# Kernel tuning notes

Hardware: AMD Instinct MI355X
Metric: run time of the kernel (lower is better)

Reference implementation:

```python
import jax, jax.numpy as jnp
import numpy as np


def _run_stacked_lstm(x, init_hc, params):
    """x: [B,T,E]; init_hc: tuple of (h,c) per layer; params: tuple of (W,U,b) per layer.
    Keras LSTMCell gate order: i, f, g(candidate), o; sigmoid recurrent act, tanh act."""
    def step(carry, xt):
        inp = xt
        new = []
        for (h, c), (W, U, b) in zip(carry, params):
            z = inp @ W + h @ U + b                      # [B, 4*units]
            i, f, g, o = jnp.split(z, 4, axis=-1)
            c2 = jax.nn.sigmoid(f) * c + jax.nn.sigmoid(i) * jnp.tanh(g)
            h2 = jax.nn.sigmoid(o) * jnp.tanh(c2)
            new.append((h2, c2))
            inp = h2                                     # feed to next layer
        return tuple(new), inp
    carry, ys = jax.lax.scan(step, init_hc, jnp.swapaxes(x, 0, 1))
    return jnp.swapaxes(ys, 0, 1), carry                 # [B,T,units], final states


def setup_inputs() -> dict:
    key = jax.random.key(0)
    ks = jax.random.split(key, 20)
    B, T, V, E, H, L = 16, 64, 32000, 512, 512, 2
    s = 0.02
    inp = {
        'ids_1': jax.random.randint(ks[0], (B, T), 0, V),
        'ids_2': jax.random.randint(ks[1], (B, T), 0, V),
        'init_state': jax.random.normal(ks[2], (L, B, H), jnp.float32),
        'emb': jax.random.normal(ks[3], (V, E), jnp.float32) * s,
        'W1_0': jax.random.normal(ks[4], (E, 4 * H), jnp.float32) * s,
        'U1_0': jax.random.normal(ks[5], (H, 4 * H), jnp.float32) * s,
        'b1_0': jnp.zeros((4 * H,), jnp.float32),
        'W1_1': jax.random.normal(ks[6], (H, 4 * H), jnp.float32) * s,
        'U1_1': jax.random.normal(ks[7], (H, 4 * H), jnp.float32) * s,
        'b1_1': jnp.zeros((4 * H,), jnp.float32),
        'W2_0': jax.random.normal(ks[8], (E, 8 * H), jnp.float32) * s,
        'U2_0': jax.random.normal(ks[9], (2 * H, 8 * H), jnp.float32) * s,
        'b2_0': jnp.zeros((8 * H,), jnp.float32),
        'W2_1': jax.random.normal(ks[10], (2 * H, 8 * H), jnp.float32) * s,
        'U2_1': jax.random.normal(ks[11], (2 * H, 8 * H), jnp.float32) * s,
        'b2_1': jnp.zeros((8 * H,), jnp.float32),
        'Wp1': jax.random.normal(ks[12], (H, V), jnp.float32) * s,
        'bp1': jnp.zeros((V,), jnp.float32),
        'Wp2': jax.random.normal(ks[13], (2 * H, V), jnp.float32) * s,
        'bp2': jnp.zeros((V,), jnp.float32),
    }
    return inp


def reference(ids_1, ids_2, init_state, emb,
              W1_0, U1_0, b1_0, W1_1, U1_1, b1_1,
              W2_0, U2_0, b2_0, W2_1, U2_1, b2_1,
              Wp1, bp1, Wp2, bp2):
    L = init_state.shape[0]
    e1 = emb[ids_1]                                       # [B,T,E]
    e2 = emb[ids_2]
    # RNN1: initial (h,c) both set to init_state per layer
    init1 = tuple((init_state[l], init_state[l]) for l in range(L))
    p1 = ((W1_0, U1_0, b1_0), (W1_1, U1_1, b1_1))
    out1, st1 = _run_stacked_lstm(e1, init1, p1)
    logits1 = out1 @ Wp1 + bp1                            # [B,T,V]
    # RNN2: initial h = concat(init, h1_final), c = concat(init, c1_final)
    init2 = tuple((jnp.concatenate([init_state[l], st1[l][0]], axis=1),
                   jnp.concatenate([init_state[l], st1[l][1]], axis=1))
                  for l in range(L))
    p2 = ((W2_0, U2_0, b2_0), (W2_1, U2_1, b2_1))
    out2, _ = _run_stacked_lstm(e2, init2, p2)
    logits2 = out2 @ Wp2 + bp2                            # [B,T,V]
    return (logits1, logits2)
```

## Files before the change

### kernel.cpp

```cpp
#include <hip/hip_runtime.h>
#include <hip/hip_bf16.h>

#define B_ 16
#define T_ 64
#define E_ 512
#define H_ 512
#define V_ 32000

typedef __attribute__((ext_vector_type(4))) float f32x4;
typedef __attribute__((ext_vector_type(8))) short s16x8;

__device__ __forceinline__ float sigm(float x){ return 1.0f/(1.0f + __expf(-x)); }

__device__ __forceinline__ unsigned short f2bf(float x){
  unsigned int u = __float_as_uint(x);
  return (unsigned short)((u + 0x7FFFu + ((u>>16)&1u)) >> 16);
}

__device__ __forceinline__ unsigned load_coh(const unsigned* p){
  unsigned v;
  asm volatile("global_load_dword %0, %1, off sc0 sc1\n\ts_waitcnt vmcnt(0)"
               : "=v"(v) : "v"(p) : "memory");
  return v;
}
__device__ __forceinline__ void store_coh16(unsigned short* p, unsigned v){
  asm volatile("global_store_short %0, %1, off sc0 sc1" :: "v"(p), "v"(v) : "memory");
}
__device__ __forceinline__ void store_cohf(float* p, float v){
  asm volatile("global_store_dword %0, %1, off sc0 sc1" :: "v"(p), "v"(v) : "memory");
}
__device__ __forceinline__ void store_cohu(unsigned* p, unsigned v){
  asm volatile("global_store_dword %0, %1, off sc0 sc1" :: "v"(p), "v"(v) : "memory");
}

__device__ __forceinline__ void gbar3(unsigned* barb, unsigned bi1, int nblk,
                                      bool det, int myblk){
  asm volatile("s_waitcnt vmcnt(0)" ::: "memory");
  __syncthreads();
  const int tid = threadIdx.x;
  if(tid == 0) store_cohu(barb + (size_t)myblk*16, bi1);
  if(det){
    if(tid < nblk){
      const unsigned* fp = barb + (size_t)tid*16;
      while(load_coh(fp) < bi1) __builtin_amdgcn_s_sleep(1);
    }
    __syncthreads();
    if(tid < 8) store_cohu(barb + 4096 + (size_t)tid*16, bi1);
  } else {
    if(tid == 0){
      const unsigned* gp = barb + 4096 + (size_t)(myblk & 7)*16;
      while(load_coh(gp) < bi1) __builtin_amdgcn_s_sleep(1);
    }
  }
  __syncthreads();
}

__global__ void k_barinit(unsigned* bar){
  int i = blockIdx.x*256 + threadIdx.x;
  if(i < 16384) bar[i] = 0u;
}

__global__ void k_gather(const int* __restrict__ ids, const float* __restrict__ emb,
                         unsigned short* __restrict__ out){
  const int row = blockIdx.x;
  const int id  = ids[row];
  float4 v = *(const float4*)(emb + (size_t)id*E_ + threadIdx.x*4);
  ushort4 o;
  o.x = f2bf(v.x); o.y = f2bf(v.y); o.z = f2bf(v.z); o.w = f2bf(v.w);
  *(ushort4*)(out + (size_t)row*E_ + threadIdx.x*4) = o;
}

__device__ __forceinline__ void tcvt_dev(const float* __restrict__ in,
    unsigned short* __restrict__ out, int N, int Hp, int Kfull, int koff, int swz,
    int bx, int by, float (*tile)[33]){
  const int n0 = bx*32, k0 = by*32;
  const int x = threadIdx.x & 31, y = threadIdx.x >> 5;
  __syncthreads();
  #pragma unroll
  for(int i=0;i<4;i++){
    int k = y + i*8;
    tile[k][x] = in[(size_t)(k0+k)*N + n0 + x];
  }
  __syncthreads();
  #pragma unroll
  for(int i=0;i<4;i++){
    int nl = y + i*8;
    int n  = n0 + nl;
    int p  = Hp ? ((n % Hp)*4 + n / Hp) : n;
    int kk = koff + k0 + x;
    size_t idx;
    if(swz){
      int k2 = kk*2;
      int slot = ((k2>>4)&7) ^ (p&7);
      idx = (size_t)p*Kfull + (((k2 & ~127) | (slot<<4) | (k2 & 15)) >> 1);
    } else {
      idx = (size_t)p*Kfull + kk;
    }
    out[idx] = f2bf(tile[x][nl]);
  }
}

__global__ __launch_bounds__(256)
void k_tcvt(const float* __restrict__ in, unsigned short* __restrict__ out,
            int N, int Hp, int Kfull, int koff, int swz){
  __shared__ float tile[32][33];
  tcvt_dev(in, out, N, Hp, Kfull, koff, swz, blockIdx.x, blockIdx.y, tile);
}

__device__ __forceinline__ void tcvtw_dev(const float* __restrict__ in,
    unsigned short* __restrict__ out, int N, int K, int bx, int by,
    float (*tile)[257]){
  const int tid = threadIdx.x;
  const int n0 = bx*256, k0 = by*32;
  const int row = tid >> 3, nc = (tid & 7)*32;
  __syncthreads();
  #pragma unroll
  for(int j=0;j<8;j++){
    float4 v = *(const float4*)(in + (size_t)(k0+row)*N + n0 + nc + j*4);
    *(float4*)&tile[row][nc + j*4] = v;
  }
  __syncthreads();
  __align__(16) unsigned short vals[32];
  #pragma unroll
  for(int k=0;k<32;k++) vals[k] = f2bf(tile[k][tid]);
  unsigned short* op = out + (size_t)(n0+tid)*K + k0;
  #pragma unroll
  for(int j=0;j<4;j++)
    *(uint4*)(op + j*8) = *(const uint4*)&vals[j*8];
}

__global__ void k_bpack(const float* __restrict__ b, float* __restrict__ out, int H, int N){
  int p = blockIdx.x*256 + threadIdx.x;
  if(p < N) out[p] = b[(p&3)*H + (p>>2)];
}

__global__ void k_init1(const float* __restrict__ init_state,
                        unsigned short* h0i, float* c0i, unsigned short* h1i, float* c1i){
  int i = blockIdx.x*256 + threadIdx.x;
  if(i >= B_*H_) return;
  float v0 = init_state[i];
  float v1 = init_state[B_*H_ + i];
  h0i[i] = f2bf(v0); c0i[i] = v0;
  h1i[i] = f2bf(v1); c1i[i] = v1;
}

__global__ void k_init2(const float* __restrict__ init_state,
                        const unsigned short* __restrict__ h0seq1,
                        const unsigned short* __restrict__ h1seq1,
                        const float* __restrict__ c0f1, const float* __restrict__ c1f1,
                        unsigned short* h20i, unsigned short* h21i,
                        float* c20i, float* c21i){
  const int l = blockIdx.y;
  int i = blockIdx.x*256 + threadIdx.x;
  if(i >= B_*2*H_) return;
  const int r = i >> 10, j = i & 1023;
  unsigned short* ho = l ? h21i : h20i;
  float* co = l ? c21i : c20i;
  if(j < H_){
    float v = init_state[(size_t)l*B_*H_ + r*H_ + j];
    ho[i] = f2bf(v); co[i] = v;
  } else {
    const unsigned short* hs = l ? h1seq1 : h0seq1;
    const float* cf = l ? c1f1 : c0f1;
    ho[i] = hs[(size_t)((T_-1)*B_ + r)*H_ + (j - H_)];
    co[i] = cf[r*H_ + (j - H_)];
  }
}

__device__ __forceinline__ void mm_tile(const unsigned short* __restrict__ A,
    const unsigned short* __restrict__ Bt, const float* __restrict__ bias,
    float* __restrict__ C, int N, int K, int bm, int bn,
    unsigned short* As, unsigned short* Bs, int remap){
  const int tid = threadIdx.x;
  const int lane = tid & 63, w = tid >> 6;
  const int wm = (w>>1)*64, wn = (w&1)*64;
  const int l15 = lane & 15, kg = lane >> 4;
  f32x4 acc[4][4] = {};
  for(int k0=0; k0<K; k0+=64){
    __syncthreads();
    #pragma unroll
    for(int ch=0; ch<4; ch++){
      int off = ch*4096 + tid*16;
      int row = off >> 7;
      int s   = ((off >> 4) & 7) ^ (row & 7);
      __builtin_amdgcn_global_load_lds(
        (const __attribute__((address_space(1))) unsigned int*)(A + (size_t)(bm+row)*K + k0 + s*8),
        (__attribute__((address_space(3))) unsigned int*)((char*)As + off), 16, 0, 0);
    }
    #pragma unroll
    for(int ch=0; ch<4; ch++){
      int off = ch*4096 + tid*16;
      int row = off >> 7;
      int s   = ((off >> 4) & 7) ^ (row & 7);
      __builtin_amdgcn_global_load_lds(
        (const __attribute__((address_space(1))) unsigned int*)(Bt + (size_t)(bn+row)*K + k0 + s*8),
        (__attribute__((address_space(3))) unsigned int*)((char*)Bs + off), 16, 0, 0);
    }
    __syncthreads();
    #pragma unroll
    for(int q=0;q<2;q++){
      s16x8 af[4], bf[4];
      #pragma unroll
      for(int mt=0;mt<4;mt++){
        int row = wm + mt*16 + l15;
        int s = (q*4 + kg) ^ (row & 7);
        af[mt] = *(const s16x8*)(As + row*64 + s*8);
      }
      #pragma unroll
      for(int nt=0;nt<4;nt++){
        int row = wn + nt*16 + l15;
        int s = (q*4 + kg) ^ (row & 7);
        bf[nt] = *(const s16x8*)(Bs + row*64 + s*8);
      }
      #pragma unroll
      for(int mt=0;mt<4;mt++)
        #pragma unroll
        for(int nt=0;nt<4;nt++)
          acc[mt][nt] = __builtin_amdgcn_mfma_f32_16x16x32_bf16(af[mt], bf[nt], acc[mt][nt], 0, 0, 0);
    }
  }
  #pragma unroll
  for(int mt=0;mt<4;mt++){
    #pragma unroll
    for(int nt=0;nt<4;nt++){
      int col = bn + wn + nt*16 + l15;
      float bv = bias ? bias[col] : 0.f;
      #pragma unroll
      for(int e=0;e<4;e++){
        int row = bm + wm + mt*16 + kg*4 + e;
        int orow = remap ? ((row & 15)*T_ + (row >> 4)) : row;
        C[(size_t)orow*N + col] = acc[mt][nt][e] + bv;
      }
    }
  }
}

template<int BF32>
__global__ __launch_bounds__(256)
void k_mm(const unsigned short* __restrict__ A, const void* __restrict__ Bsrc,
          const float* __restrict__ bias, float* __restrict__ C,
          int M, int N, int K, int remap, int bm0){
  __shared__ __align__(16) unsigned short As[128*64];
  __shared__ __align__(16) unsigned short Bs[128*64];
  if(!BF32){
    mm_tile(A, (const unsigned short*)Bsrc, bias, C, N, K,
            bm0 + blockIdx.y*128, blockIdx.x*128, As, Bs, remap);
    return;
  }
  const int tid = threadIdx.x;
  const int lane = tid & 63, w = tid >> 6;
  const int wm = (w>>1)*64, wn = (w&1)*64;
  const int bm = bm0 + blockIdx.y*128, bn = blockIdx.x*128;
  const int l15 = lane & 15, kg = lane >> 4;
  f32x4 acc[4][4] = {};
  for(int k0=0; k0<K; k0+=64){
    __syncthreads();
    #pragma unroll
    for(int ch=0; ch<4; ch++){
      int off = ch*4096 + tid*16;
      int row = off >> 7;
      int s   = ((off >> 4) & 7) ^ (row & 7);
      __builtin_amdgcn_global_load_lds(
        (const __attribute__((address_space(1))) unsigned int*)(A + (size_t)(bm+row)*K + k0 + s*8),
        (__attribute__((address_space(3))) unsigned int*)((char*)As + off), 16, 0, 0);
    }
    {
      const float* Bf = (const float*)Bsrc;
      #pragma unroll
      for(int i=0;i<8;i++){
        int kl = (tid>>5) + i*8;
        int nl = (tid&31)*4;
        float4 v = *(const float4*)(Bf + (size_t)(k0+kl)*N + bn + nl);
        int slot = kl >> 3, kb = kl & 7;
        float vv[4] = {v.x, v.y, v.z, v.w};
        #pragma unroll
        for(int jj=0;jj<4;jj++){
          int n = nl + jj;
          Bs[n*64 + ((slot ^ (n&7))*8) + kb] = f2bf(vv[jj]);
        }
      }
    }
    __syncthreads();
    #pragma unroll
    for(int q=0;q<2;q++){
      s16x8 af[4], bf[4];
      #pragma unroll
      for(int mt=0;mt<4;mt++){
        int row = wm + mt*16 + l15;
        int s = (q*4 + kg) ^ (row & 7);
        af[mt] = *(const s16x8*)(As + row*64 + s*8);
      }
      #pragma unroll
      for(int nt=0;nt<4;nt++){
        int row = wn + nt*16 + l15;
        int s = (q*4 + kg) ^ (row & 7);
        bf[nt] = *(const s16x8*)(Bs + row*64 + s*8);
      }
      #pragma unroll
      for(int mt=0;mt<4;mt++)
        #pragma unroll
        for(int nt=0;nt<4;nt++)
          acc[mt][nt] = __builtin_amdgcn_mfma_f32_16x16x32_bf16(af[mt], bf[nt], acc[mt][nt], 0, 0, 0);
    }
  }
  #pragma unroll
  for(int mt=0;mt<4;mt++){
    #pragma unroll
    for(int nt=0;nt<4;nt++){
      int col = bn + wn + nt*16 + l15;
      float bv = bias ? bias[col] : 0.f;
      #pragma unroll
      for(int e=0;e<4;e++){
        int row = bm + wm + mt*16 + kg*4 + e;
        int orow = remap ? ((row & 15)*T_ + (row >> 4)) : row;
        C[(size_t)orow*N + col] = acc[mt][nt][e] + bv;
      }
    }
  }
}

template<int C, int K, int LAYER, int HU, int TB>
__device__ __forceinline__ void rnn_body(
    unsigned short* __restrict__ Uld, float* __restrict__ zp,
    const unsigned short* __restrict__ Uslice,
    const float* __restrict__ xw0, const float* __restrict__ bpk,
    const unsigned short* __restrict__ h0init, const unsigned short* __restrict__ h1init,
    const float* __restrict__ cinit,
    unsigned short* __restrict__ h0seq, unsigned short* __restrict__ h1seq,
    float* __restrict__ cfin, unsigned* bar, int cb, int nblk, bool det, int myblk)
{
  constexpr int KW = K/4, KS = KW/32, FR = C/16, UB = C/4;
  constexpr int K2 = K*2;
  constexpr int ITEMS = 16*UB;
  const int tid = threadIdx.x;
  const int lane = tid & 63, w = tid >> 6;
  const int l15 = lane & 15, kg = lane >> 4;

  constexpr int CP = (C*K2)/4096;
  #pragma unroll
  for(int i=0;i<CP;i++){
    __builtin_amdgcn_global_load_lds(
      (const __attribute__((address_space(1))) unsigned int*)((const char*)Uslice + i*4096 + tid*16),
      (__attribute__((address_space(3))) unsigned int*)((char*)Uld + i*4096 + tid*16), 16, 0, 0);
  }
  const int base_p = cb*C;
  const int base_u = cb*UB;
  float4 bvr = make_float4(0.f,0.f,0.f,0.f);
  int er = 0, eu = 0;
  if(tid < ITEMS){ er = tid / UB; eu = tid - er*UB; bvr = *(const float4*)(bpk + base_p + eu*4); }
  float creg = 0.f;
  unsigned short* hseqW = LAYER ? h1seq : h0seq;

  int cbyte[FR], cx[FR];
  #pragma unroll
  for(int f=0;f<FR;f++){ int c = f*16 + l15; cbyte[f] = c*K2; cx[f] = (c&7)<<4; }

  __syncthreads();

  for(int it = 0; it <= T_; ++it){
    const bool active = LAYER ? (it >= 1) : (it < T_);
    const int t = LAYER ? it-1 : it;
    if(active){
      const unsigned short* asrc;
      if constexpr(LAYER == 0){
        asrc = (t == 0) ? (h0init + l15*HU)
             : (h0seq + ((size_t)(TB ? ((t-1)*B_ + l15) : (l15*T_ + (t-1))))*HU);
      } else {
        if(w < 2){
          asrc = h0seq + ((size_t)(TB ? (t*B_ + l15) : (l15*T_ + t)))*HU;
        } else {
          asrc = ((t == 0) ? (h1init + l15*HU)
               : (h1seq + ((size_t)(TB ? ((t-1)*B_ + l15) : (l15*T_ + (t-1))))*HU)) - HU;
        }
      }
      f32x4 acc[FR];
      #pragma unroll
      for(int f=0;f<FR;f++) acc[f] = (f32x4){0.f,0.f,0.f,0.f};
      #pragma unroll
      for(int s=0;s<KS;s++){
        const int kel = w*KW + s*32 + kg*8;
        s16x8 a = *(const s16x8*)(asrc + kel);
        const int kb  = kel*2;
        const int kch = kb & ~127;
        const int ksl = (kb >> 4) & 7;
        #pragma unroll
        for(int f=0;f<FR;f++){
          const int ad = cbyte[f] + kch + ((ksl<<4) ^ cx[f]);
          s16x8 b = *(const s16x8*)((const char*)Uld + ad);
          acc[f] = __builtin_amdgcn_mfma_f32_16x16x32_bf16(a, b, acc[f], 0, 0, 0);
        }
      }
      #pragma unroll
      for(int f=0;f<FR;f++)
        #pragma unroll
        for(int e=0;e<4;e++)
          zp[(w*16 + kg*4 + e)*68 + f*16 + l15] = acc[f][e];
    }
    __syncthreads();
    if(active && tid < ITEMS){
      float4 z0 = *(const float4*)(zp + (     er)*68 + eu*4);
      float4 z1 = *(const float4*)(zp + (16 + er)*68 + eu*4);
      float4 z2 = *(const float4*)(zp + (32 + er)*68 + eu*4);
      float4 z3 = *(const float4*)(zp + (48 + er)*68 + eu*4);
      float si = z0.x+z1.x+z2.x+z3.x + bvr.x;
      float sf = z0.y+z1.y+z2.y+z3.y + bvr.y;
      float sg = z0.z+z1.z+z2.z+z3.z + bvr.z;
      float so = z0.w+z1.w+z2.w+z3.w + bvr.w;
      if constexpr(LAYER == 0){
        float4 xv = *(const float4*)(xw0 + ((size_t)(er*T_ + t))*(4*HU) + base_p + eu*4);
        si += xv.x; sf += xv.y; sg += xv.z; so += xv.w;
      }
      float cin = (t == 0) ? cinit[er*HU + base_u + eu] : creg;
      float c2 = sigm(sf)*cin + sigm(si)*tanhf(sg);
      float h2 = sigm(so)*tanhf(c2);
      creg = c2;
      size_t hrow = TB ? ((size_t)(t*B_ + er)) : ((size_t)(er*T_ + t));
      store_coh16(&hseqW[hrow*HU + base_u + eu], (unsigned)f2bf(h2));
      if(t == T_-1) store_cohf(&cfin[er*HU + base_u + eu], c2);
    }
    if(it < T_) gbar3(bar, (unsigned)(it+1), nblk, det, myblk);
  }
  asm volatile("s_waitcnt vmcnt(0)" ::: "memory");
  __syncthreads();
  if(tid == 0) store_cohu(bar + (size_t)myblk*16, (unsigned)(T_+1));
}

__global__ __launch_bounds__(256, 1)
void k_rnn1m(const unsigned short* __restrict__ Ut0, const unsigned short* __restrict__ WU1,
    const float* __restrict__ xw0, const float* __restrict__ bpk0, const float* __restrict__ bpk1,
    const unsigned short* __restrict__ h0init, const unsigned short* __restrict__ h1init,
    const float* __restrict__ c0init, const float* __restrict__ c1init,
    unsigned short* __restrict__ h0seq, unsigned short* __restrict__ h1seq,
    float* __restrict__ c0fin, float* __restrict__ c1fin, unsigned* bar,
    const int* __restrict__ ids2, const float* __restrict__ emb, unsigned short* __restrict__ ebuf2,
    const float* __restrict__ b2_0, const float* __restrict__ b2_1,
    float* __restrict__ bpk20, float* __restrict__ bpk21,
    const float* __restrict__ U2_0, unsigned short* __restrict__ ut0_2,
    const float* __restrict__ W2_0, unsigned short* __restrict__ wtmp2,
    const float* __restrict__ W2_1, const float* __restrict__ U2_1, unsigned short* __restrict__ wu1_2,
    const float* __restrict__ Wp1, unsigned short* __restrict__ wpT1,
    const float* __restrict__ Wp2, unsigned short* __restrict__ wpT2,
    const float* __restrict__ bp1, float* __restrict__ out1,
    float* __restrict__ xw2buf, int wide)
{
  constexpr int HU = 512, C0 = 64, C1 = 64;
  constexpr int NB0 = 4*HU/C0;
  constexpr int NRNN = NB0 + 4*HU/C1;
  constexpr int NP = 96;
  constexpr int NJ = 96;
  __shared__ __align__(16) unsigned short Uld[65536];
  __shared__ __align__(16) float zred[64*68];
  const int blk = blockIdx.x;
  const int tid = threadIdx.x;
  if(blk < NB0){
    rnn_body<C0, HU, 0, HU, 1>(Uld, zred, Ut0 + (size_t)blk*C0*HU, xw0, bpk0,
        h0init, h1init, c0init, h0seq, h1seq, c0fin, bar, blk, NRNN, blk==0, blk);
  } else if(blk < NRNN){
    rnn_body<C1, 2*HU, 1, HU, 1>(Uld, zred, WU1 + (size_t)(blk-NB0)*C1*2*HU, nullptr, bpk1,
        h0init, h1init, c1init, h0seq, h1seq, c1fin, bar, blk-NB0, NRNN, false, blk);
  } else if(blk < NRNN + NP){
    const int q = blk - NRNN;
    float (*tile)[33]   = (float(*)[33])Uld;
    float (*tile2)[257] = (float(*)[257])Uld;
    unsigned short* As = Uld;
    unsigned short* Bs = Uld + 8192;
    if(wide){
      for(int j = q; j < 2000; j += NP)
        tcvtw_dev(Wp1, wpT1, 32000, 512, j%125, j/125, tile2);
    }
    __syncthreads();
    __threadfence();
    if(tid == 0)
      __hip_atomic_fetch_add(bar + 5136, 1u, __ATOMIC_RELAXED, __HIP_MEMORY_SCOPE_AGENT);
    const int J0 = 512, J1 = J0+32, J2 = J1+4096, J3 = J2+2048, J4 = J3+4096, J5 = J4+4096;
    const int J6 = wide ? (J5 + 4000) : J5;
    for(int j = q; j < J6; j += NP){
      if(j < J0){
        int row = j*2 + (tid>>7);
        int id = ids2[row];
        float4 v = *(const float4*)(emb + (size_t)id*E_ + (tid&127)*4);
        ushort4 o; o.x=f2bf(v.x); o.y=f2bf(v.y); o.z=f2bf(v.z); o.w=f2bf(v.w);
        *(ushort4*)(ebuf2 + (size_t)row*E_ + (tid&127)*4) = o;
      } else if(j < J1){
        int jj = j - J0;
        const float* b = (jj < 16) ? b2_0 : b2_1;
        float* o = (jj < 16) ? bpk20 : bpk21;
        int p = (jj & 15)*256 + tid;
        o[p] = b[(p&3)*1024 + (p>>2)];
      } else if(j < J2){
        int r = j - J1; tcvt_dev(U2_0, ut0_2, 4096, 1024, 1024, 0, 1, r%128, r/128, tile);
      } else if(j < J3){
        int r = j - J2; tcvt_dev(W2_0, wtmp2, 4096, 1024, 512, 0, 0, r%128, r/128, tile);
      } else if(j < J4){
        int r = j - J3; tcvt_dev(W2_1, wu1_2, 4096, 1024, 2048, 0, 1, r%128, r/128, tile);
      } else if(j < J5){
        int r = j - J4; tcvt_dev(U2_1, wu1_2, 4096, 1024, 2048, 1024, 1, r%128, r/128, tile);
      } else {
        int r = j - J5; tcvtw_dev(Wp2, wpT2, 32000, 1024, r%125, r/125, tile2);
      }
    }
    __syncthreads();
    __threadfence();
    if(tid == 0)
      __hip_atomic_fetch_add(bar + 5152, 1u, __ATOMIC_RELAXED, __HIP_MEMORY_SCOPE_AGENT);
    if(tid == 0){
      while(load_coh(bar + 5152) < (unsigned)NP) __builtin_amdgcn_s_sleep(8);
    }
    __syncthreads();
    if(xw2buf){
      for(int t2 = q; t2 < 256; t2 += NP)
        mm_tile(ebuf2, wtmp2, nullptr, xw2buf, 4096, 512, (t2>>5)*128, (t2&31)*128, As, Bs, 0);
    }
  } else {
    if(!wide) return;
    const int q2 = blk - NRNN - NP;
    unsigned short* As = Uld;
    unsigned short* Bs = Uld + 8192;
    volatile int* rdy = (volatile int*)((char*)Uld + 128000);
    if(tid == 0){
      while(load_coh(bar + 5136) < (unsigned)NP) __builtin_amdgcn_s_sleep(8);
    }
    __syncthreads();
    for(int g = 0; g < 8; ++g){
      const unsigned req = 8u*(unsigned)g + 9u;
      for(;;){
        if(tid == 0) *rdy = 1;
        __syncthreads();
        if(tid < 32){
          if(load_coh(bar + (size_t)(NB0 + tid)*16) < req) *rdy = 0;
        }
        __syncthreads();
        if(*rdy) break;
        __builtin_amdgcn_s_sleep(16);
      }
      for(int n = q2; n < 250; n += NJ)
        mm_tile(h1seq, wpT1, bp1, out1, V_, 512, g*128, n*128, As, Bs, 1);
    }
  }
}

template<int HU, int C0, int C1>
__global__ __launch_bounds__(256, 1)
void k_rnn(const unsigned short* __restrict__ Ut0, const unsigned short* __restrict__ WU1,
           const float* __restrict__ xw0, const float* __restrict__ bpk0, const float* __restrict__ bpk1,
           const unsigned short* __restrict__ h0init, const unsigned short* __restrict__ h1init,
           const float* __restrict__ c0init, const float* __restrict__ c1init,
           unsigned short* __restrict__ h0seq, unsigned short* __restrict__ h1seq,
           float* __restrict__ c0fin, float* __restrict__ c1fin, unsigned* bar)
{
  constexpr int NB0 = 4*HU/C0;
  constexpr int UMAXE = (C0*HU > C1*2*HU) ? C0*HU : C1*2*HU;
  __shared__ __align__(16) unsigned short Uld[UMAXE];
  __shared__ __align__(16) float zred[64*68];
  const int nblk = gridDim.x;
  const bool det = (blockIdx.x == 0);
  const int blk = blockIdx.x;
  if(blk < NB0)
    rnn_body<C0, HU, 0, HU, 1>(Uld, zred, Ut0 + (size_t)blk*C0*HU, xw0, bpk0,
                               h0init, h1init, c0init, h0seq, h1seq, c0fin, bar, blk, nblk, det, blk);
  else
    rnn_body<C1, 2*HU, 1, HU, 1>(Uld, zred, WU1 + (size_t)(blk-NB0)*C1*2*HU, nullptr, bpk1,
                               h0init, h1init, c1init, h0seq, h1seq, c1fin, bar, blk-NB0, nblk, det, blk);
}

extern "C" void kernel_launch(void* const* d_in, const int* in_sizes, int n_in,
                              void* d_out, int out_size, void* d_ws, size_t ws_size,
                              hipStream_t stream){
  const int*   ids1 = (const int*)d_in[0];
  const int*   ids2 = (const int*)d_in[1];
  const float* init = (const float*)d_in[2];
  const float* emb  = (const float*)d_in[3];
  const float* W1_0 = (const float*)d_in[4];
  const float* U1_0 = (const float*)d_in[5];
  const float* b1_0 = (const float*)d_in[6];
  const float* W1_1 = (const float*)d_in[7];
  const float* U1_1 = (const float*)d_in[8];
  const float* b1_1 = (const float*)d_in[9];
  const float* W2_0 = (const float*)d_in[10];
  const float* U2_0 = (const float*)d_in[11];
  const float* b2_0 = (const float*)d_in[12];
  const float* W2_1 = (const float*)d_in[13];
  const float* U2_1 = (const float*)d_in[14];
  const float* b2_1 = (const float*)d_in[15];
  const float* Wp1  = (const float*)d_in[16];
  const float* bp1  = (const float*)d_in[17];
  const float* Wp2  = (const float*)d_in[18];
  const float* bp2  = (const float*)d_in[19];
  float* out1 = (float*)d_out;
  float* out2 = out1 + (size_t)B_*T_*V_;

  char* base = (char*)d_ws;
  float*          xw    = (float*)(base);
  unsigned short* ut0_1 = (unsigned short*)(base + (16u<<20));
  unsigned short* wu1_1 = (unsigned short*)(base + (18u<<20));
  unsigned short* ut0_2 = (unsigned short*)(base + (22u<<20));
  unsigned short* wu1_2 = (unsigned short*)(base + (30u<<20));
  unsigned short* wtmp  = (unsigned short*)(base + (46u<<20));
  unsigned short* ebuf  = (unsigned short*)(base + (50u<<20));
  unsigned short* h0s1  = (unsigned short*)(base + (51u<<20));
  unsigned short* h1s1  = (unsigned short*)(base + (52u<<20));
  unsigned short* h0s2  = (unsigned short*)(base + (53u<<20));
  unsigned short* h1s2  = (unsigned short*)(base + (55u<<20));
  char* M = base + (57u<<20);
  unsigned short* h0i1 = (unsigned short*)(M);
  unsigned short* h1i1 = (unsigned short*)(M + 16384);
  float* c0i1 = (float*)(M + 32768);
  float* c1i1 = (float*)(M + 65536);
  unsigned short* h2i0 = (unsigned short*)(M + 98304);
  unsigned short* h2i1 = (unsigned short*)(M + 131072);
  float* c2i0 = (float*)(M + 163840);
  float* c2i1 = (float*)(M + 229376);
  float* c0f1 = (float*)(M + 294912);
  float* c1f1 = (float*)(M + 327680);
  float* c0f2 = (float*)(M + 360448);
  float* c1f2 = (float*)(M + 425984);
  float* bpk10 = (float*)(M + 491520);
  float* bpk11 = (float*)(M + 499712);
  float* bpk20 = (float*)(M + 507904);
  float* bpk21 = (float*)(M + 524288);
  unsigned* bar1 = (unsigned*)(M + 540672);
  unsigned* bar2 = (unsigned*)(M + 540672 + 32768);
  unsigned short* wpT1 = (unsigned short*)(base + (58u<<20));
  unsigned short* wpT2 = (unsigned short*)(base + (90u<<20));
  float*          xw2  = (float*)(base + (153u<<20));
  const size_t NEED_W  = ((size_t)90u<<20) + (size_t)V_*1024*2;
  const size_t NEED_W2 = ((size_t)169u<<20);
  const bool wide  = ws_size >= NEED_W;
  const bool wide2 = ws_size >= NEED_W2;
  float* xw2p = (wide && wide2) ? xw2 : xw;

  k_barinit<<<dim3(64), dim3(256), 0, stream>>>(bar1);

  k_init1<<<dim3(32), dim3(256), 0, stream>>>(init, h0i1, c0i1, h1i1, c1i1);
  k_gather<<<dim3(B_*T_), dim3(128), 0, stream>>>(ids1, emb, ebuf);
  k_tcvt<<<dim3(64, 16), dim3(256), 0, stream>>>(U1_0, ut0_1, 2048, 512, 512, 0, 1);
  k_tcvt<<<dim3(64, 16), dim3(256), 0, stream>>>(W1_0, wtmp,  2048, 512, 512, 0, 0);
  k_tcvt<<<dim3(64, 16), dim3(256), 0, stream>>>(W1_1, wu1_1, 2048, 512, 1024, 0, 1);
  k_tcvt<<<dim3(64, 16), dim3(256), 0, stream>>>(U1_1, wu1_1, 2048, 512, 1024, 512, 1);
  k_bpack<<<dim3(8),  dim3(256), 0, stream>>>(b1_0, bpk10, 512, 2048);
  k_bpack<<<dim3(8),  dim3(256), 0, stream>>>(b1_1, bpk11, 512, 2048);
  k_mm<0><<<dim3(16, 8), dim3(256), 0, stream>>>(ebuf, wtmp, nullptr, xw, 1024, 2048, 512, 0, 0);

  k_rnn1m<<<dim3(256), dim3(256), 0, stream>>>(ut0_1, wu1_1, xw, bpk10, bpk11,
      h0i1, h1i1, c0i1, c1i1, h0s1, h1s1, c0f1, c1f1, bar1,
      ids2, emb, ebuf, b2_0, b2_1, bpk20, bpk21,
      U2_0, ut0_2, W2_0, wtmp, W2_1, U2_1, wu1_2,
      Wp1, wpT1, Wp2, wpT2, bp1, out1,
      (wide && wide2) ? xw2 : nullptr, (int)wide);

  if(!wide){
    k_mm<1><<<dim3(250, 8), dim3(256), 0, stream>>>(h1s1, Wp1, bp1, out1, 1024, V_, 512, 1, 0);
  }
  if(!wide || !wide2){
    k_mm<0><<<dim3(32, 8), dim3(256), 0, stream>>>(ebuf, wtmp, nullptr, xw, 1024, 4096, 512, 0, 0);
  }
  k_init2<<<dim3(64, 2), dim3(256), 0, stream>>>(init, h0s1, h1s1, c0f1, c1f1,
                                                 h2i0, h2i1, c2i0, c2i1);

  k_rnn<1024, 64, 32><<<dim3(192), dim3(256), 0, stream>>>(ut0_2, wu1_2, xw2p, bpk20, bpk21,
      h2i0, h2i1, c2i0, c2i1, h0s2, h1s2, c0f2, c1f2, bar2);

  if(wide){
    k_mm<0><<<dim3(250, 8), dim3(256), 0, stream>>>(h1s2, wpT2, bp2, out2, 1024, V_, 1024, 1, 0);
  } else {
    k_mm<1><<<dim3(250, 8), dim3(256), 0, stream>>>(h1s2, Wp2, bp2, out2, 1024, V_, 1024, 1, 0);
  }
}
```

Baseline: 872.1 us.

## Replace centralized grid barrier with per-block flag polling and layer-scoped dependencies

Removes the two-level grid barrier, in which a detector block gathered all flags and then broadcast a release. Each RNN block now publishes its own step counter and, at the start of every step, polls the flags it depends on directly. Layer-0 blocks wait only on layer-0 blocks, while layer-1 blocks wait on all RNN blocks. This drops one hop of global-memory latency per step and loosens coupling between the layers, at the cost of more polling traffic from 64 threads per block.

```diff
diff --git a/kernel.cpp b/kernel.cpp
--- a/kernel.cpp
+++ b/kernel.cpp
@@ -31,28 +31,6 @@
 }
 __device__ __forceinline__ void store_cohu(unsigned* p, unsigned v){
   asm volatile("global_store_dword %0, %1, off sc0 sc1" :: "v"(p), "v"(v) : "memory");
-}
-
-__device__ __forceinline__ void gbar3(unsigned* barb, unsigned bi1, int nblk,
-                                      bool det, int myblk){
-  asm volatile("s_waitcnt vmcnt(0)" ::: "memory");
-  __syncthreads();
-  const int tid = threadIdx.x;
-  if(tid == 0) store_cohu(barb + (size_t)myblk*16, bi1);
-  if(det){
-    if(tid < nblk){
-      const unsigned* fp = barb + (size_t)tid*16;
-      while(load_coh(fp) < bi1) __builtin_amdgcn_s_sleep(1);
-    }
-    __syncthreads();
-    if(tid < 8) store_cohu(barb + 4096 + (size_t)tid*16, bi1);
-  } else {
-    if(tid == 0){
-      const unsigned* gp = barb + 4096 + (size_t)(myblk & 7)*16;
-      while(load_coh(gp) < bi1) __builtin_amdgcn_s_sleep(1);
-    }
-  }
-  __syncthreads();
 }
 
 __global__ void k_barinit(unsigned* bar){
@@ -327,7 +305,7 @@
     const unsigned short* __restrict__ h0init, const unsigned short* __restrict__ h1init,
     const float* __restrict__ cinit,
     unsigned short* __restrict__ h0seq, unsigned short* __restrict__ h1seq,
-    float* __restrict__ cfin, unsigned* bar, int cb, int nblk, bool det, int myblk)
+    float* __restrict__ cfin, unsigned* bar, int cb, int nb0, int nrnn, int myblk)
 {
   constexpr int KW = K/4, KS = KW/32, FR = C/16, UB = C/4;
   constexpr int K2 = K*2;
@@ -358,6 +336,18 @@
   __syncthreads();
 
   for(int it = 0; it <= T_; ++it){
+    if(it > 0){
+      if(tid < 64){
+        const int fmax = (LAYER == 0) ? nb0 : nrnn;
+        for(int f = tid; f < fmax; f += 64){
+          const unsigned* fp = bar + (size_t)f*16;
+          if(load_coh(fp) < (unsigned)it){
+            while(load_coh(fp) < (unsigned)it) __builtin_amdgcn_s_sleep(4);
+          }
+        }
+      }
+      __syncthreads();
+    }
     const bool active = LAYER ? (it >= 1) : (it < T_);
     const int t = LAYER ? it-1 : it;
     if(active){
@@ -418,11 +408,10 @@
       store_coh16(&hseqW[hrow*HU + base_u + eu], (unsigned)f2bf(h2));
       if(t == T_-1) store_cohf(&cfin[er*HU + base_u + eu], c2);
     }
-    if(it < T_) gbar3(bar, (unsigned)(it+1), nblk, det, myblk);
-  }
-  asm volatile("s_waitcnt vmcnt(0)" ::: "memory");
-  __syncthreads();
-  if(tid == 0) store_cohu(bar + (size_t)myblk*16, (unsigned)(T_+1));
+    asm volatile("s_waitcnt vmcnt(0)" ::: "memory");
+    __syncthreads();
+    if(tid == 0) store_cohu(bar + (size_t)myblk*16, (unsigned)(it+1));
+  }
 }
 
 __global__ __launch_bounds__(256, 1)
@@ -454,10 +443,10 @@
   const int tid = threadIdx.x;
   if(blk < NB0){
     rnn_body<C0, HU, 0, HU, 1>(Uld, zred, Ut0 + (size_t)blk*C0*HU, xw0, bpk0,
-        h0init, h1init, c0init, h0seq, h1seq, c0fin, bar, blk, NRNN, blk==0, blk);
+        h0init, h1init, c0init, h0seq, h1seq, c0fin, bar, blk, NB0, NRNN, blk);
   } else if(blk < NRNN){
     rnn_body<C1, 2*HU, 1, HU, 1>(Uld, zred, WU1 + (size_t)(blk-NB0)*C1*2*HU, nullptr, bpk1,
-        h0init, h1init, c1init, h0seq, h1seq, c1fin, bar, blk-NB0, NRNN, false, blk);
+        h0init, h1init, c1init, h0seq, h1seq, c1fin, bar, blk-NB0, NB0, NRNN, blk);
   } else if(blk < NRNN + NP){
     const int q = blk - NRNN;
     float (*tile)[33]   = (float(*)[33])Uld;
@@ -549,18 +538,17 @@
            float* __restrict__ c0fin, float* __restrict__ c1fin, unsigned* bar)
 {
   constexpr int NB0 = 4*HU/C0;
+  constexpr int NRNN = NB0 + 4*HU/C1;
   constexpr int UMAXE = (C0*HU > C1*2*HU) ? C0*HU : C1*2*HU;
   __shared__ __align__(16) unsigned short Uld[UMAXE];
   __shared__ __align__(16) float zred[64*68];
-  const int nblk = gridDim.x;
-  const bool det = (blockIdx.x == 0);
   const int blk = blockIdx.x;
   if(blk < NB0)
     rnn_body<C0, HU, 0, HU, 1>(Uld, zred, Ut0 + (size_t)blk*C0*HU, xw0, bpk0,
-                               h0init, h1init, c0init, h0seq, h1seq, c0fin, bar, blk, nblk, det, blk);
+                               h0init, h1init, c0init, h0seq, h1seq, c0fin, bar, blk, NB0, NRNN, blk);
   else
     rnn_body<C1, 2*HU, 1, HU, 1>(Uld, zred, WU1 + (size_t)(blk-NB0)*C1*2*HU, nullptr, bpk1,
-                               h0init, h1init, c1init, h0seq, h1seq, c1fin, bar, blk-NB0, nblk, det, blk);
+                               h0init, h1init, c1init, h0seq, h1seq, c1fin, bar, blk-NB0, NB0, NRNN, blk);
 }
 
 extern "C" void kernel_launch(void* const* d_in, const int* in_sizes, int n_in,
```

Measured after the change: 869.2 us. No clear change (-0.3%).
